# Kernel optimization log

Hardware: AMD Instinct MI355X
Metric: run time of the kernel (lower is better)

The kernel has to match this reference:

```python
import jax, jax.numpy as jnp
import numpy as np

SEQ_LEN = 2049  # conf.SEQ_LEN; sequence axis of inputs is SEQ_LEN - 1
BATCH = 1024
N_FEAT = 11

# Static lookup table of type masks (rows 0..7 per the if/elif ladder; row 8 = all-False 'else').
# Rows 4..6 are placeholders: they are replaced by the dynamic prefix-count branch.
_TYPE_TABLE = np.zeros((9, 8), dtype=bool)
_TYPE_TABLE[0] = [0, 1, 0, 0, 0, 0, 0, 0]
_TYPE_TABLE[1] = [0, 1, 1, 0, 0, 0, 0, 0]
_TYPE_TABLE[2] = [0, 0, 0, 0, 1, 0, 0, 0]
_TYPE_TABLE[3] = [0, 0, 0, 1, 1, 1, 1, 1]
_TYPE_TABLE[7] = [0, 0, 0, 0, 0, 0, 0, 1]

_MASK_NO_TIMESIGN = np.array([0, 0, 0, 0, 0, 1, 0, 0], dtype=bool)  # time_sign_occurrences == 0
_MASK_NO_TEMPO    = np.array([0, 0, 0, 0, 0, 0, 1, 0], dtype=bool)  # tempo_occurrences == 0
_MASK_FULL        = np.array([0, 0, 0, 1, 1, 1, 1, 1], dtype=bool)  # both present -> same as type 3


def setup_inputs() -> dict:
    key = jax.random.key(0)
    inputs = jax.random.randint(key, (BATCH, SEQ_LEN - 1, N_FEAT), 0, 8, dtype=jnp.int32)
    return {"inputs": inputs}


def reference(inputs) -> jnp.ndarray:
    gt = inputs[:, :, 0]                       # [B, L] token types, L = SEQ_LEN - 1
    B, L = gt.shape

    # Base masks from the static per-type table ('else' -> row 8, all False).
    table = jnp.asarray(_TYPE_TABLE)
    base = table[jnp.clip(gt, 0, 8)]           # [B, L, 8]

    # Prefix counts: for token i, count types over positions j with j <= i + 1 (inclusive).
    is5 = (gt == 5).astype(jnp.int32)
    is6 = (gt == 6).astype(jnp.int32)
    c5 = jnp.cumsum(is5, axis=1)               # inclusive cumsum
    c6 = jnp.cumsum(is6, axis=1)
    idx = jnp.minimum(jnp.arange(L) + 1, L - 1)  # position i looks at prefix up to min(i+1, L-1)
    cnt5 = c5[:, idx]                           # [B, L] time_sign occurrences
    cnt6 = c6[:, idx]                           # [B, L] tempo occurrences

    # Dynamic branch for token types 4..6.
    no_ts = (cnt5 == 0)[..., None]              # [B, L, 1]
    no_tp = (cnt6 == 0)[..., None]
    dyn = jnp.where(no_ts, jnp.asarray(_MASK_NO_TIMESIGN),
                    jnp.where(no_tp, jnp.asarray(_MASK_NO_TEMPO), jnp.asarray(_MASK_FULL)))  # [B, L, 8]

    cond456 = ((gt >= 4) & (gt <= 6))[..., None]
    masks = jnp.where(cond456, dyn, base)       # [B, L, 8] bool
    return masks
```

## Files before the change

kernel.cpp:

```cpp
#include <hip/hip_runtime.h>


#define SEQ_L 2048
#define NF 11
#define BLOCK 512
#define PASSES 11
#define OPASS 8

__global__ __launch_bounds__(BLOCK)
void mask_type_prob_kernel(const int* __restrict__ in, int* __restrict__ out) {
    __shared__ int s_gt[SEQ_L];
    __shared__ unsigned s_f5, s_f6;

    const int b   = blockIdx.x;
    const int tid = threadIdx.x;

    if (tid == 0) { s_f5 = 0xFFFFFFFFu; s_f6 = 0xFFFFFFFFu; }
    __syncthreads();

    const int4* rowv = (const int4*)(in + (size_t)b * SEQ_L * NF);

    int4 v[PASSES];
    #pragma unroll
    for (int p = 0; p < PASSES; ++p) {
        v[p] = rowv[tid + p * BLOCK];
    }
    __builtin_amdgcn_sched_barrier(0);

    unsigned f5 = 0xFFFFFFFFu, f6 = 0xFFFFFFFFu;
    #pragma unroll
    for (int p = 0; p < PASSES; ++p) {
        const int i4 = tid + p * BLOCK;
        const int j  = i4 * 4;
        const int mi  = (j + 10) / 11;
        const int pos = mi * 11 - j;
        if (pos < 4) {
            const int gv = (pos == 0) ? v[p].x : (pos == 1) ? v[p].y
                         : (pos == 2) ? v[p].z : v[p].w;
            s_gt[mi] = gv;
            if (gv == 5) f5 = min(f5, (unsigned)mi);
            if (gv == 6) f6 = min(f6, (unsigned)mi);
        }
    }

    #pragma unroll
    for (int off = 32; off >= 1; off >>= 1) {
        f5 = min(f5, (unsigned)__shfl_xor((int)f5, off, 64));
        f6 = min(f6, (unsigned)__shfl_xor((int)f6, off, 64));
    }
    if ((tid & 63) == 0) {
        if (f5 != 0xFFFFFFFFu) atomicMin(&s_f5, f5);
        if (f6 != 0xFFFFFFFFu) atomicMin(&s_f6, f6);
    }
    __syncthreads();

    const unsigned first5 = s_f5;
    const unsigned first6 = s_f6;

    const unsigned long long pack = 0x80000000F8100602ULL;

    int4* orowv = (int4*)(out + (size_t)b * SEQ_L * 8);

    #pragma unroll
    for (int k = 0; k < OPASS; ++k) {
        const int c    = tid + k * BLOCK;
        const int t    = c >> 1;
        const int half = c & 1;
        const int gv   = s_gt[t];
        unsigned m;
        if (gv >= 4 && gv <= 6) {
            const unsigned idx = (unsigned)((t + 1 < SEQ_L - 1) ? (t + 1) : (SEQ_L - 1));
            m = (first5 > idx) ? 0x20u : ((first6 > idx) ? 0x40u : 0xF8u);
        } else {
            const int gc = gv < 0 ? 0 : (gv > 8 ? 8 : gv);
            m = (gc >= 8) ? 0u : (unsigned)((pack >> (gc * 8)) & 0xFFu);
        }
        const unsigned nib = half ? (m >> 4) : m;
        int4 w;
        w.x = (int)((nib >> 0) & 1u);
        w.y = (int)((nib >> 1) & 1u);
        w.z = (int)((nib >> 2) & 1u);
        w.w = (int)((nib >> 3) & 1u);
        orowv[c] = w;
    }
}

extern "C" void kernel_launch(void* const* d_in, const int* in_sizes, int n_in,
                              void* d_out, int out_size, void* d_ws, size_t ws_size,
                              hipStream_t stream) {
    const int* in = (const int*)d_in[0];
    int* out = (int*)d_out;
    const int batch = in_sizes[0] / (SEQ_L * NF);
    mask_type_prob_kernel<<<batch, BLOCK, 0, stream>>>(in, out);
}
```

Before: 153.0 us.

## Split fused per-row kernel into init, grid-stride scan, and emit kernels

Replaces the single one-block-per-row kernel with three launches: an init kernel for per-row first-occurrence indices, a flat grid-stride scan that extracts token types into a workspace and records first 5/6 positions with global atomicMin, and a flat emit kernel that writes the mask output. The aim is to decouple the grid from the batch size and give more parallelism and memory-level concurrency. The cost is two extra launches, a global round trip for the gt array, and contended global atomics. Batch size is now hardcoded instead of derived from the input size.

```diff
diff --git a/kernel.cpp b/kernel.cpp
--- a/kernel.cpp
+++ b/kernel.cpp
@@ -3,74 +3,64 @@
 
 #define SEQ_L 2048
 #define NF 11
-#define BLOCK 512
-#define PASSES 11
-#define OPASS 8
+#define BATCH 1024
+#define IN_CHUNKS (BATCH * SEQ_L * NF / 4)
+#define ROW_CHUNKS (SEQ_L * NF / 4)
+#define OUT_CHUNKS (BATCH * SEQ_L * 8 / 4)
+#define K1_GRID 2816
+#define K1_PASSES 8
+#define K2_GRID 4096
+#define K2_PASSES 4
 
-__global__ __launch_bounds__(BLOCK)
-void mask_type_prob_kernel(const int* __restrict__ in, int* __restrict__ out) {
-    __shared__ int s_gt[SEQ_L];
-    __shared__ unsigned s_f5, s_f6;
+__global__ __launch_bounds__(256)
+void mask_init_kernel(unsigned* __restrict__ firsts) {
+    const int i = blockIdx.x * 256 + threadIdx.x;
+    if (i < 2 * BATCH) firsts[i] = 0xFFFFFFFFu;
+}
 
-    const int b   = blockIdx.x;
-    const int tid = threadIdx.x;
-
-    if (tid == 0) { s_f5 = 0xFFFFFFFFu; s_f6 = 0xFFFFFFFFu; }
-    __syncthreads();
-
-    const int4* rowv = (const int4*)(in + (size_t)b * SEQ_L * NF);
-
-    int4 v[PASSES];
+__global__ __launch_bounds__(256)
+void mask_scan_kernel(const int* __restrict__ in, int* __restrict__ gt_out,
+                      unsigned* __restrict__ first5, unsigned* __restrict__ first6) {
+    const int base = blockIdx.x * 256 + threadIdx.x;
+    const int stride = K1_GRID * 256;
+    const int4* inv = (const int4*)in;
     #pragma unroll
-    for (int p = 0; p < PASSES; ++p) {
-        v[p] = rowv[tid + p * BLOCK];
-    }
-    __builtin_amdgcn_sched_barrier(0);
-
-    unsigned f5 = 0xFFFFFFFFu, f6 = 0xFFFFFFFFu;
-    #pragma unroll
-    for (int p = 0; p < PASSES; ++p) {
-        const int i4 = tid + p * BLOCK;
-        const int j  = i4 * 4;
-        const int mi  = (j + 10) / 11;
-        const int pos = mi * 11 - j;
+    for (int p = 0; p < K1_PASSES; ++p) {
+        const int c = base + p * stride;
+        const int4 v = inv[c];
+        const int row = c / ROW_CHUNKS;
+        const int jr  = (c - row * ROW_CHUNKS) * 4;
+        const int mi  = (jr + 10) / 11;
+        const int pos = mi * 11 - jr;
         if (pos < 4) {
-            const int gv = (pos == 0) ? v[p].x : (pos == 1) ? v[p].y
-                         : (pos == 2) ? v[p].z : v[p].w;
-            s_gt[mi] = gv;
-            if (gv == 5) f5 = min(f5, (unsigned)mi);
-            if (gv == 6) f6 = min(f6, (unsigned)mi);
+            const int gv = (pos == 0) ? v.x : (pos == 1) ? v.y
+                         : (pos == 2) ? v.z : v.w;
+            gt_out[row * SEQ_L + mi] = gv;
+            if (gv == 5) atomicMin(&first5[row], (unsigned)mi);
+            if (gv == 6) atomicMin(&first6[row], (unsigned)mi);
         }
     }
+}
 
+__global__ __launch_bounds__(256)
+void mask_emit_kernel(const int* __restrict__ gt, const unsigned* __restrict__ first5,
+                      const unsigned* __restrict__ first6, int* __restrict__ out) {
+    const int base = blockIdx.x * 256 + threadIdx.x;
+    const int stride = K2_GRID * 256;
+    const unsigned long long pack = 0x80000000F8100602ULL;
+    int4* outv = (int4*)out;
     #pragma unroll
-    for (int off = 32; off >= 1; off >>= 1) {
-        f5 = min(f5, (unsigned)__shfl_xor((int)f5, off, 64));
-        f6 = min(f6, (unsigned)__shfl_xor((int)f6, off, 64));
-    }
-    if ((tid & 63) == 0) {
-        if (f5 != 0xFFFFFFFFu) atomicMin(&s_f5, f5);
-        if (f6 != 0xFFFFFFFFu) atomicMin(&s_f6, f6);
-    }
-    __syncthreads();
-
-    const unsigned first5 = s_f5;
-    const unsigned first6 = s_f6;
-
-    const unsigned long long pack = 0x80000000F8100602ULL;
-
-    int4* orowv = (int4*)(out + (size_t)b * SEQ_L * 8);
-
-    #pragma unroll
-    for (int k = 0; k < OPASS; ++k) {
-        const int c    = tid + k * BLOCK;
-        const int t    = c >> 1;
+    for (int p = 0; p < K2_PASSES; ++p) {
+        const int c   = base + p * stride;
+        const int tg  = c >> 1;
         const int half = c & 1;
-        const int gv   = s_gt[t];
+        const int row = tg >> 11;
+        const int t   = tg & (SEQ_L - 1);
+        const int gv  = gt[tg];
         unsigned m;
         if (gv >= 4 && gv <= 6) {
             const unsigned idx = (unsigned)((t + 1 < SEQ_L - 1) ? (t + 1) : (SEQ_L - 1));
-            m = (first5 > idx) ? 0x20u : ((first6 > idx) ? 0x40u : 0xF8u);
+            m = (first5[row] > idx) ? 0x20u : ((first6[row] > idx) ? 0x40u : 0xF8u);
         } else {
             const int gc = gv < 0 ? 0 : (gv > 8 ? 8 : gv);
             m = (gc >= 8) ? 0u : (unsigned)((pack >> (gc * 8)) & 0xFFu);
@@ -81,7 +71,7 @@
         w.y = (int)((nib >> 1) & 1u);
         w.z = (int)((nib >> 2) & 1u);
         w.w = (int)((nib >> 3) & 1u);
-        orowv[c] = w;
+        outv[c] = w;
     }
 }
 
@@ -90,6 +80,13 @@
                               hipStream_t stream) {
     const int* in = (const int*)d_in[0];
     int* out = (int*)d_out;
-    const int batch = in_sizes[0] / (SEQ_L * NF);
-    mask_type_prob_kernel<<<batch, BLOCK, 0, stream>>>(in, out);
+
+    unsigned* firsts = (unsigned*)d_ws;
+    unsigned* first5 = firsts;
+    unsigned* first6 = firsts + BATCH;
+    int* gt = (int*)(firsts + 2 * BATCH);
+
+    mask_init_kernel<<<(2 * BATCH + 255) / 256, 256, 0, stream>>>(firsts);
+    mask_scan_kernel<<<K1_GRID, 256, 0, stream>>>(in, gt, first5, first6);
+    mask_emit_kernel<<<K2_GRID, 256, 0, stream>>>(gt, first5, first6, out);
 }
```

Result: slower. 429.0 us (+180.4%).

## Process two batch rows per block, prefetching second row during first row's output

Applied to the files above, without the earlier changes.

Each block now handles two batch rows. The loads for the second row are issued before the first row's output is written, so the read latency overlaps the store phase. The grid is halved, which lowers parallelism across CUs. Batch must be even, and the first row's loads are no longer batched ahead with a sched_barrier.

```diff
diff --git a/kernel.cpp b/kernel.cpp
--- a/kernel.cpp
+++ b/kernel.cpp
@@ -7,60 +7,9 @@
 #define PASSES 11
 #define OPASS 8
 
-__global__ __launch_bounds__(BLOCK)
-void mask_type_prob_kernel(const int* __restrict__ in, int* __restrict__ out) {
-    __shared__ int s_gt[SEQ_L];
-    __shared__ unsigned s_f5, s_f6;
-
-    const int b   = blockIdx.x;
-    const int tid = threadIdx.x;
-
-    if (tid == 0) { s_f5 = 0xFFFFFFFFu; s_f6 = 0xFFFFFFFFu; }
-    __syncthreads();
-
-    const int4* rowv = (const int4*)(in + (size_t)b * SEQ_L * NF);
-
-    int4 v[PASSES];
-    #pragma unroll
-    for (int p = 0; p < PASSES; ++p) {
-        v[p] = rowv[tid + p * BLOCK];
-    }
-    __builtin_amdgcn_sched_barrier(0);
-
-    unsigned f5 = 0xFFFFFFFFu, f6 = 0xFFFFFFFFu;
-    #pragma unroll
-    for (int p = 0; p < PASSES; ++p) {
-        const int i4 = tid + p * BLOCK;
-        const int j  = i4 * 4;
-        const int mi  = (j + 10) / 11;
-        const int pos = mi * 11 - j;
-        if (pos < 4) {
-            const int gv = (pos == 0) ? v[p].x : (pos == 1) ? v[p].y
-                         : (pos == 2) ? v[p].z : v[p].w;
-            s_gt[mi] = gv;
-            if (gv == 5) f5 = min(f5, (unsigned)mi);
-            if (gv == 6) f6 = min(f6, (unsigned)mi);
-        }
-    }
-
-    #pragma unroll
-    for (int off = 32; off >= 1; off >>= 1) {
-        f5 = min(f5, (unsigned)__shfl_xor((int)f5, off, 64));
-        f6 = min(f6, (unsigned)__shfl_xor((int)f6, off, 64));
-    }
-    if ((tid & 63) == 0) {
-        if (f5 != 0xFFFFFFFFu) atomicMin(&s_f5, f5);
-        if (f6 != 0xFFFFFFFFu) atomicMin(&s_f6, f6);
-    }
-    __syncthreads();
-
-    const unsigned first5 = s_f5;
-    const unsigned first6 = s_f6;
-
+__device__ __forceinline__ void emit_row(const int* s_gt, unsigned first5,
+                                         unsigned first6, int4* orowv, int tid) {
     const unsigned long long pack = 0x80000000F8100602ULL;
-
-    int4* orowv = (int4*)(out + (size_t)b * SEQ_L * 8);
-
     #pragma unroll
     for (int k = 0; k < OPASS; ++k) {
         const int c    = tid + k * BLOCK;
@@ -85,11 +34,91 @@
     }
 }
 
+__global__ __launch_bounds__(BLOCK)
+void mask_type_prob_kernel(const int* __restrict__ in, int* __restrict__ out) {
+    __shared__ int s_gt[2][SEQ_L];
+    __shared__ unsigned s_f[4];
+
+    const int tid = threadIdx.x;
+    const int b0  = blockIdx.x * 2;
+    const int b1  = b0 + 1;
+
+    if (tid < 4) s_f[tid] = 0xFFFFFFFFu;
+    __syncthreads();
+
+    const int4* row0 = (const int4*)(in + (size_t)b0 * SEQ_L * NF);
+    const int4* row1 = (const int4*)(in + (size_t)b1 * SEQ_L * NF);
+
+    unsigned f5 = 0xFFFFFFFFu, f6 = 0xFFFFFFFFu;
+    #pragma unroll
+    for (int p = 0; p < PASSES; ++p) {
+        const int i4 = tid + p * BLOCK;
+        const int4 v = row0[i4];
+        const int j  = i4 * 4;
+        const int mi  = (j + 10) / 11;
+        const int pos = mi * 11 - j;
+        if (pos < 4) {
+            const int gv = (pos == 0) ? v.x : (pos == 1) ? v.y
+                         : (pos == 2) ? v.z : v.w;
+            s_gt[0][mi] = gv;
+            if (gv == 5) f5 = min(f5, (unsigned)mi);
+            if (gv == 6) f6 = min(f6, (unsigned)mi);
+        }
+    }
+    #pragma unroll
+    for (int off = 32; off >= 1; off >>= 1) {
+        f5 = min(f5, (unsigned)__shfl_xor((int)f5, off, 64));
+        f6 = min(f6, (unsigned)__shfl_xor((int)f6, off, 64));
+    }
+    if ((tid & 63) == 0) {
+        if (f5 != 0xFFFFFFFFu) atomicMin(&s_f[0], f5);
+        if (f6 != 0xFFFFFFFFu) atomicMin(&s_f[1], f6);
+    }
+    __syncthreads();
+    const unsigned f5_0 = s_f[0], f6_0 = s_f[1];
+
+    int4 w[PASSES];
+    #pragma unroll
+    for (int p = 0; p < PASSES; ++p) {
+        w[p] = row1[tid + p * BLOCK];
+    }
+
+    emit_row(s_gt[0], f5_0, f6_0, (int4*)(out + (size_t)b0 * SEQ_L * 8), tid);
+
+    f5 = 0xFFFFFFFFu; f6 = 0xFFFFFFFFu;
+    #pragma unroll
+    for (int p = 0; p < PASSES; ++p) {
+        const int i4 = tid + p * BLOCK;
+        const int j  = i4 * 4;
+        const int mi  = (j + 10) / 11;
+        const int pos = mi * 11 - j;
+        if (pos < 4) {
+            const int gv = (pos == 0) ? w[p].x : (pos == 1) ? w[p].y
+                         : (pos == 2) ? w[p].z : w[p].w;
+            s_gt[1][mi] = gv;
+            if (gv == 5) f5 = min(f5, (unsigned)mi);
+            if (gv == 6) f6 = min(f6, (unsigned)mi);
+        }
+    }
+    #pragma unroll
+    for (int off = 32; off >= 1; off >>= 1) {
+        f5 = min(f5, (unsigned)__shfl_xor((int)f5, off, 64));
+        f6 = min(f6, (unsigned)__shfl_xor((int)f6, off, 64));
+    }
+    if ((tid & 63) == 0) {
+        if (f5 != 0xFFFFFFFFu) atomicMin(&s_f[2], f5);
+        if (f6 != 0xFFFFFFFFu) atomicMin(&s_f[3], f6);
+    }
+    __syncthreads();
+
+    emit_row(s_gt[1], s_f[2], s_f[3], (int4*)(out + (size_t)b1 * SEQ_L * 8), tid);
+}
+
 extern "C" void kernel_launch(void* const* d_in, const int* in_sizes, int n_in,
                               void* d_out, int out_size, void* d_ws, size_t ws_size,
                               hipStream_t stream) {
     const int* in = (const int*)d_in[0];
     int* out = (int*)d_out;
     const int batch = in_sizes[0] / (SEQ_L * NF);
-    mask_type_prob_kernel<<<batch, BLOCK, 0, stream>>>(in, out);
+    mask_type_prob_kernel<<<batch / 2, BLOCK, 0, stream>>>(in, out);
 }
```

New measurement: 155.3 us. Within noise of the previous version (+1.5%).
